# Optimization experiments

Measured on AMD Instinct MI355X. Metric: run time of the kernel, lower is better.

Reference implementation:

```python
import jax, jax.numpy as jnp
import numpy as np

N, E, B = 4096, 4096, 128  # nodes, edges, graphs


def _param(key, shape, scale):
    return jax.random.normal(key, shape, dtype=jnp.float32) * scale


def setup_inputs() -> dict:
    key = jax.random.key(0)
    ks = jax.random.split(key, 32)
    inp = {
        "x": jax.random.normal(ks[0], (N, 37), dtype=jnp.float32),
        "edge_index": jax.random.randint(ks[1], (2, E), 0, N),
        "edge_attr": jax.random.uniform(ks[2], (E, 5), dtype=jnp.float32),
        "batch": jnp.sort(jax.random.randint(ks[3], (N,), 0, B)),
        # NNConv 1: edge-MLP 5->512->37*128, root [37,128]
        "nn1_w1": _param(ks[4], (5, 512), 0.3),
        "nn1_b1": jnp.zeros((512,), jnp.float32),
        "nn1_w2": _param(ks[5], (512, 37 * 128), 0.01),
        "nn1_b2": jnp.zeros((37 * 128,), jnp.float32),
        "root1": _param(ks[6], (37, 128), 0.1),
        "bias1": jnp.zeros((128,), jnp.float32),
        # NNConv 2: edge-MLP 5->128->128*256, root [128,256]
        "nn2_w1": _param(ks[7], (5, 128), 0.3),
        "nn2_b1": jnp.zeros((128,), jnp.float32),
        "nn2_w2": _param(ks[8], (128, 128 * 256), 0.005),
        "nn2_b2": jnp.zeros((128 * 256,), jnp.float32),
        "root2": _param(ks[9], (128, 256), 0.05),
        "bias2": jnp.zeros((256,), jnp.float32),
        # NNConv 3: edge-MLP 5->128->256*256, root [256,256]
        "nn3_w1": _param(ks[10], (5, 128), 0.3),
        "nn3_b1": jnp.zeros((128,), jnp.float32),
        "nn3_w2": _param(ks[11], (128, 256 * 256), 0.005),
        "nn3_b2": jnp.zeros((256 * 256,), jnp.float32),
        "root3": _param(ks[12], (256, 256), 0.05),
        "bias3": jnp.zeros((256,), jnp.float32),
        # readout MLP
        "fc1_w": _param(ks[13], (256, 128), 0.06),
        "fc1_b": jnp.zeros((128,), jnp.float32),
        "fc2_w": _param(ks[14], (128, 64), 0.09),
        "fc2_b": jnp.zeros((64,), jnp.float32),
        "fc3_w": _param(ks[15], (64, 1), 0.12),
        "fc3_b": jnp.zeros((1,), jnp.float32),
    }
    return inp


def _nnconv(x, src, dst, edge_attr, w1, b1, w2, b2, root, bias, cin, cout):
    # edge MLP -> per-edge weight matrix [E, cin, cout]
    h = jax.nn.relu(edge_attr @ w1 + b1)
    W = (h @ w2 + b2).reshape(-1, cin, cout)
    # gather source features, per-edge matvec, scatter-add to targets
    msg = jnp.einsum('ei,eio->eo', x[src], W)          # [E, cout]
    agg = jax.ops.segment_sum(msg, dst, num_segments=x.shape[0])
    return agg + x @ root + bias


def _segment_mean(x, seg, num_segments):
    s = jax.ops.segment_sum(x, seg, num_segments=num_segments)
    cnt = jax.ops.segment_sum(jnp.ones((x.shape[0],), x.dtype), seg,
                              num_segments=num_segments)
    return s / jnp.maximum(cnt, 1.0)[:, None]


def reference(x, edge_index, edge_attr, batch,
              nn1_w1, nn1_b1, nn1_w2, nn1_b2, root1, bias1,
              nn2_w1, nn2_b1, nn2_w2, nn2_b2, root2, bias2,
              nn3_w1, nn3_b1, nn3_w2, nn3_b2, root3, bias3,
              fc1_w, fc1_b, fc2_w, fc2_b, fc3_w, fc3_b):
    src, dst = edge_index[0], edge_index[1]
    h = jax.nn.elu(_nnconv(x, src, dst, edge_attr, nn1_w1, nn1_b1, nn1_w2,
                           nn1_b2, root1, bias1, 37, 128))
    h = jax.nn.elu(_nnconv(h, src, dst, edge_attr, nn2_w1, nn2_b1, nn2_w2,
                           nn2_b2, root2, bias2, 128, 256))
    h = jax.nn.elu(_nnconv(h, src, dst, edge_attr, nn3_w1, nn3_b1, nn3_w2,
                           nn3_b2, root3, bias3, 256, 256))
    g = _segment_mean(h, batch, B)                     # [B, 256]
    g = jax.nn.elu(g @ fc1_w + fc1_b)
    g = jax.nn.elu(g @ fc2_w + fc2_b)
    g = g @ fc3_w + fc3_b
    return g.reshape(-1)
```

## Files before the change

### kernel.cpp

```cpp
#include <hip/hip_runtime.h>
#include <cstdint>
#include <cstddef>

typedef float f32x4 __attribute__((ext_vector_type(4)));
typedef _Float16 f16x8 __attribute__((ext_vector_type(8)));
typedef _Float16 f16x4 __attribute__((ext_vector_type(4)));

__device__ __forceinline__ float elu_f(float x) { return x > 0.f ? x : expm1f(x); }

__device__ __forceinline__ void gload_lds16(const void* g, void* l)
{
    __builtin_amdgcn_global_load_lds(
        (const __attribute__((address_space(1))) void*)g,
        (__attribute__((address_space(3))) void*)l,
        16, 0, 0);
}

__global__ __launch_bounds__(256)
void edge_mlp_kernel(const float* __restrict__ ea,
                     const int* __restrict__ dst, int* __restrict__ cnt,
                     const float* __restrict__ w1a, const float* __restrict__ b1a, _Float16* __restrict__ h1T,
                     const float* __restrict__ w1b, const float* __restrict__ b1b, _Float16* __restrict__ h2T,
                     const float* __restrict__ w1c, const float* __restrict__ b1c, _Float16* __restrict__ h3T,
                     int E)
{
    const int e0  = blockIdx.x * 64;
    const int tid = threadIdx.x;
    const int el  = tid & 63;
    const int cg  = tid >> 6;
    if (tid < 64) atomicAdd(&cnt[dst[e0 + tid]], 1);
    __shared__ float a[64][5];
    for (int i = tid; i < 320; i += 256) a[i / 5][i % 5] = ea[e0 * 5 + i];
    __syncthreads();
    float av[5];
    #pragma unroll
    for (int j = 0; j < 5; ++j) av[j] = a[el][j];

    #pragma unroll 4
    for (int t = 0; t < 128; ++t) {
        const int ch = t * 4 + cg;
        float s = b1a[ch];
        #pragma unroll
        for (int j = 0; j < 5; ++j) s = fmaf(av[j], w1a[j * 512 + ch], s);
        h1T[(size_t)ch * E + e0 + el] = (_Float16)fmaxf(s, 0.f);
    }
    #pragma unroll 4
    for (int t = 0; t < 32; ++t) {
        const int ch = t * 4 + cg;
        float s = b1b[ch];
        float u = b1c[ch];
        #pragma unroll
        for (int j = 0; j < 5; ++j) {
            s = fmaf(av[j], w1b[j * 128 + ch], s);
            u = fmaf(av[j], w1c[j * 128 + ch], u);
        }
        h2T[(size_t)ch * E + e0 + el] = (_Float16)fmaxf(s, 0.f);
        h3T[(size_t)ch * E + e0 + el] = (_Float16)fmaxf(u, 0.f);
    }
}

template <int CIN, int COUT, int KFTOT>
__global__ __launch_bounds__(256)
void pack_w2_kernel(const float* __restrict__ w2, const float* __restrict__ b2,
                    _Float16* __restrict__ w2h, int KH)
{
    __shared__ float tile[32][COUT + 2];
    const int bid = blockIdx.x;
    const int kh  = bid / KFTOT;
    const int c   = bid - kh * KFTOT;
    const int tid = threadIdx.x;
    const int CP  = 32 * COUT;
    for (int i = tid; i < CP; i += 256) {
        int kk = i / COUT, n = i - kk * COUT;
        int kg = c * 32 + kk;
        float v = 0.f;
        if (kg < CIN) v = (kh < KH) ? w2[((size_t)kh * CIN + kg) * COUT + n]
                                    : b2[(size_t)kg * COUT + n];
        tile[kk][n] = v;
    }
    __syncthreads();
    _Float16* outp = w2h + (size_t)bid * CP;
    for (int i = tid; i < CP; i += 256) {
        int n = i >> 5, kk = i & 31;
        int blk = (kk >> 3) ^ ((n >> 1) & 3);
        outp[n * 32 + blk * 8 + (kk & 7)] = (_Float16)tile[kk][n];
    }
}

__global__ __launch_bounds__(256)
void csr_scan_graph_kernel(const int* __restrict__ cnt, int* __restrict__ offs, int N,
                           const int* __restrict__ batch, int* __restrict__ goffs, int B,
                           int NN)
{
    __shared__ int sums[256];
    __shared__ int pref[257];
    const int tid = threadIdx.x;
    const int per = N / 256;
    int loc = 0;
    for (int i = 0; i < per; ++i) loc += cnt[tid * per + i];
    sums[tid] = loc;
    __syncthreads();
    if (tid == 0) {
        int s = 0; pref[0] = 0;
        for (int i = 0; i < 256; ++i) { s += sums[i]; pref[i + 1] = s; }
    }
    __syncthreads();
    int run = pref[tid];
    for (int i = 0; i < per; ++i) { offs[tid * per + i] = run; run += cnt[tid * per + i]; }
    if (tid == 255) offs[N] = run;
    for (int g = tid; g <= B; g += 256) {
        int lo = 0, hi = NN;
        while (lo < hi) { int mid = (lo + hi) >> 1; if (batch[mid] < g) lo = mid + 1; else hi = mid; }
        goffs[g] = lo;
    }
}

__global__ __launch_bounds__(256)
void csr_fill_kernel(const int* __restrict__ dst, const int* __restrict__ offs,
                     int* __restrict__ cur, int* __restrict__ eid, int E)
{
    int e = blockIdx.x * 256 + threadIdx.x;
    if (e < E) {
        int d = dst[e];
        int p = offs[d] + atomicAdd(&cur[d], 1);
        eid[p] = e;
    }
}

template <int KH, int CIN, int COUT, int KFTOT, int CSPLIT, int NY>
__global__ __launch_bounds__(256, 4)
void msg_mfma_kernel(const float* __restrict__ xin,
                     const _Float16* __restrict__ hT,
                     const _Float16* __restrict__ w2h,
                     const int* __restrict__ src,
                     _Float16* __restrict__ part,
                     int E, int khg_per)
{
    constexpr int BM = 128;
    constexpr int KF = KFTOT / CSPLIT;

    __shared__ __align__(16) _Float16 bsh[2][KF][64][32];
    __shared__ _Float16 s_h[2][BM];
    __shared__ int s_src[BM];

    const int tid  = threadIdx.x;
    const int lane = tid & 63;
    const int w    = tid >> 6;
    const int l15  = lane & 15;
    const int lg   = lane >> 4;
    const int swb  = (l15 >> 1) & 3;

    const int nwg = gridDim.x;
    const int bid = blockIdx.x;
    const int swz = (bid & 7) * (nwg >> 3) + (bid >> 3);
    const int m    = swz & 31;
    const int rest = swz >> 5;
    const int y    = rest % NY;
    const int zz   = rest / NY;
    const int cinH = zz % CSPLIT;
    const int zkh  = zz / CSPLIT;

    const int e0  = m * BM;
    const int n0  = y * 64;
    const int k0  = cinH * KF * 32;
    const int kh0 = zkh * khg_per;
    const int kh1 = min(kh0 + khg_per, KH + 1);

    if (tid < BM) s_src[tid] = src[e0 + tid];
    __syncthreads();

    f16x8 a_[2][KF];
    #pragma unroll
    for (int mf = 0; mf < 2; ++mf) {
        const int eloc = w * 32 + mf * 16 + l15;
        const float* xrow = xin + (size_t)s_src[eloc] * CIN + k0;
        #pragma unroll
        for (int c = 0; c < KF; ++c) {
            if (CIN % 32 == 0) {
                float4 p0 = *(const float4*)(xrow + c * 32 + lg * 8);
                float4 p1 = *(const float4*)(xrow + c * 32 + lg * 8 + 4);
                a_[mf][c][0] = (_Float16)p0.x; a_[mf][c][1] = (_Float16)p0.y;
                a_[mf][c][2] = (_Float16)p0.z; a_[mf][c][3] = (_Float16)p0.w;
                a_[mf][c][4] = (_Float16)p1.x; a_[mf][c][5] = (_Float16)p1.y;
                a_[mf][c][6] = (_Float16)p1.z; a_[mf][c][7] = (_Float16)p1.w;
            } else {
                #pragma unroll
                for (int j = 0; j < 8; ++j) {
                    int kk = c * 32 + lg * 8 + j;
                    float v = (k0 + kk < CIN) ? xrow[kk] : 0.f;
                    a_[mf][c][j] = (_Float16)v;
                }
            }
        }
    }

    f32x4 msg[2][4];
    #pragma unroll
    for (int mf = 0; mf < 2; ++mf)
        #pragma unroll
        for (int nf = 0; nf < 4; ++nf) msg[mf][nf] = 0.f;

    auto stage = [&](int khg, int pp) {
        if (khg >= kh1) return;
        const size_t chunk0 = (size_t)khg * KFTOT + cinH * KF;
        const char* g = (const char*)(w2h + (chunk0 * COUT + n0) * 32) + (size_t)tid * 16;
        char* l = (char*)(&bsh[pp][0][0][0]) + (tid >> 6) * 1024;
        #pragma unroll
        for (int c = 0; c < KF; ++c)
            gload_lds16(g + (size_t)c * COUT * 64, l + c * 4096);
    };
    auto stage_h = [&](int khg) {
        if (tid < BM && khg < kh1 && khg < KH)
            s_h[khg & 1][tid] = hT[(size_t)khg * E + e0 + tid];
    };

    int p = 0;
    stage(kh0, 0);
    stage_h(kh0);

    for (int khg = kh0; khg < kh1; ++khg) {
        __syncthreads();

        stage(khg + 1, p ^ 1);
        stage_h(khg + 1);

        _Float16 hh[2];
        #pragma unroll
        for (int mf = 0; mf < 2; ++mf)
            hh[mf] = (khg < KH) ? s_h[khg & 1][w * 32 + mf * 16 + l15] : (_Float16)1.0f;

        #pragma unroll
        for (int c = 0; c < KF; ++c) {
            f16x8 Bv[4];
            #pragma unroll
            for (int nf = 0; nf < 4; ++nf)
                Bv[nf] = *(const f16x8*)&bsh[p][c][nf * 16 + l15][(lg ^ swb) * 8];
            #pragma unroll
            for (int mf = 0; mf < 2; ++mf) {
                f16x8 ah = a_[mf][c] * hh[mf];
                #pragma unroll
                for (int nf = 0; nf < 4; ++nf)
                    msg[mf][nf] = __builtin_amdgcn_mfma_f32_16x16x32_f16(ah, Bv[nf], msg[mf][nf], 0, 0, 0);
            }
        }
        p ^= 1;
    }

    _Float16* pb = part + ((size_t)zz * E + e0) * COUT + n0;
    #pragma unroll
    for (int mf = 0; mf < 2; ++mf)
        #pragma unroll
        for (int r = 0; r < 4; ++r) {
            const int row = w * 32 + mf * 16 + lg * 4 + r;
            #pragma unroll
            for (int nf = 0; nf < 4; ++nf)
                pb[(size_t)row * COUT + nf * 16 + l15] = (_Float16)msg[mf][nf][r];
        }
}

template <int CIN, int COUT, int Z>
__global__ __launch_bounds__(256)
void node_gemm_kernel(const float* __restrict__ xin,
                      const float* __restrict__ root,
                      const _Float16* __restrict__ part,
                      const int* __restrict__ offs,
                      const int* __restrict__ eid,
                      const float* __restrict__ bias,
                      float* __restrict__ out, int E)
{
    constexpr int BM  = 64;
    constexpr int BN  = 64;
    constexpr int BKI = (CIN % 32 == 0) ? 32 : 16;
    constexpr int CIN_PAD = ((CIN + BKI - 1) / BKI) * BKI;
    constexpr int CPK = CIN_PAD / BKI;
    constexpr int NROWS = BKI / 16;

    __shared__ __align__(16) float xs_t[CIN_PAD][BM];
    __shared__ __align__(16) float btile[BKI][BN];

    const int tid = threadIdx.x;
    const int tx  = tid & 15;
    const int ty  = tid >> 4;
    const int ty4 = ty * 4;
    const int tx4 = tx * 4;
    const int e0  = blockIdx.x * BM;
    const int n0  = blockIdx.y * BN;

    for (int idx = tid; idx < BM * CIN_PAD; idx += 256) {
        int mm = idx / CIN_PAD;
        int i  = idx - mm * CIN_PAD;
        float v = 0.f;
        if (i < CIN) v = xin[(size_t)(e0 + mm) * CIN + i];
        xs_t[i][mm] = v;
    }

    const int rbase = tid >> 4;
    const int nn    = (tid & 15) * 4;
    float acc[4][4] = {};
    float4 pre[NROWS];

    {
        const float* brow = root + n0;
        #pragma unroll
        for (int rr = 0; rr < NROWS; ++rr) {
            int r = rbase + rr * 16;
            float4 v = {0.f, 0.f, 0.f, 0.f};
            if (r < CIN) v = *(const float4*)(brow + (size_t)r * COUT + nn);
            pre[rr] = v;
        }
    }

    for (int c = 0; c < CPK; ++c) {
        __syncthreads();
        #pragma unroll
        for (int rr = 0; rr < NROWS; ++rr)
            *(float4*)&btile[rbase + rr * 16][nn] = pre[rr];
        __syncthreads();

        if (c + 1 < CPK) {
            int i0n = (c + 1) * BKI;
            const float* brow = root + (size_t)i0n * COUT + n0;
            #pragma unroll
            for (int rr = 0; rr < NROWS; ++rr) {
                int r = rbase + rr * 16;
                float4 v = {0.f, 0.f, 0.f, 0.f};
                if (i0n + r < CIN) v = *(const float4*)(brow + (size_t)r * COUT + nn);
                pre[rr] = v;
            }
        }

        const int i0 = c * BKI;
        #pragma unroll
        for (int ii = 0; ii < BKI; ++ii) {
            float4 xv = *(const float4*)&xs_t[i0 + ii][ty4];
            float4 bv = *(const float4*)&btile[ii][tx4];
            float av[4] = {xv.x, xv.y, xv.z, xv.w};
            float bvv[4] = {bv.x, bv.y, bv.z, bv.w};
            #pragma unroll
            for (int mm = 0; mm < 4; ++mm)
                #pragma unroll
                for (int nq = 0; nq < 4; ++nq)
                    acc[mm][nq] = fmaf(av[mm], bvv[nq], acc[mm][nq]);
        }
    }

    float bs[4];
    #pragma unroll
    for (int nq = 0; nq < 4; ++nq) bs[nq] = bias[n0 + tx4 + nq];

    #pragma unroll
    for (int mm = 0; mm < 4; ++mm) {
        const int row = e0 + ty4 + mm;
        float add[4] = {0.f, 0.f, 0.f, 0.f};
        const int b = offs[row], t = offs[row + 1];
        for (int j = b; j < t; ++j) {
            const int e = eid[j];
            #pragma unroll
            for (int z = 0; z < Z; ++z) {
                f16x4 r4 = *(const f16x4*)(part + ((size_t)z * E + e) * COUT + n0 + tx4);
                add[0] += (float)r4.x; add[1] += (float)r4.y;
                add[2] += (float)r4.z; add[3] += (float)r4.w;
            }
        }
        size_t base = (size_t)row * COUT + n0 + tx4;
        #pragma unroll
        for (int nq = 0; nq < 4; ++nq)
            out[base + nq] = elu_f(acc[mm][nq] + add[nq] + bs[nq]);
    }
}

__global__ __launch_bounds__(256)
void pool_readout_kernel(const float* __restrict__ hl3, const int* __restrict__ goffs,
                         const float* __restrict__ fc1w, const float* __restrict__ fc1b,
                         const float* __restrict__ fc2w, const float* __restrict__ fc2b,
                         const float* __restrict__ fc3w, const float* __restrict__ fc3b,
                         float* __restrict__ outp)
{
    const int g   = blockIdx.x;
    const int tid = threadIdx.x;
    __shared__ float gm[256];
    __shared__ float a1[128];
    __shared__ float a2[64];
    const int b = goffs[g], t = goffs[g + 1];
    float s = 0.f;
    for (int n = b; n < t; ++n) s += hl3[(size_t)n * 256 + tid];
    gm[tid] = s / fmaxf((float)(t - b), 1.f);
    __syncthreads();
    if (tid < 128) {
        float v = fc1b[tid];
        for (int j = 0; j < 256; ++j) v = fmaf(gm[j], fc1w[j * 128 + tid], v);
        a1[tid] = elu_f(v);
    }
    __syncthreads();
    if (tid < 64) {
        float v = fc2b[tid];
        for (int j = 0; j < 128; ++j) v = fmaf(a1[j], fc2w[j * 64 + tid], v);
        a2[tid] = elu_f(v);
    }
    __syncthreads();
    if (tid == 0) {
        float v = fc3b[0];
        for (int j = 0; j < 64; ++j) v = fmaf(a2[j], fc3w[j], v);
        outp[g] = v;
    }
}

extern "C" void kernel_launch(void* const* d_in, const int* in_sizes, int n_in,
                              void* d_out, int out_size, void* d_ws, size_t ws_size,
                              hipStream_t stream)
{
    const float* x      = (const float*)d_in[0];
    const int*   ei     = (const int*)  d_in[1];
    const float* ea     = (const float*)d_in[2];
    const int*   batch  = (const int*)  d_in[3];
    const float* nn1_w1 = (const float*)d_in[4];
    const float* nn1_b1 = (const float*)d_in[5];
    const float* nn1_w2 = (const float*)d_in[6];
    const float* nn1_b2 = (const float*)d_in[7];
    const float* root1  = (const float*)d_in[8];
    const float* bias1  = (const float*)d_in[9];
    const float* nn2_w1 = (const float*)d_in[10];
    const float* nn2_b1 = (const float*)d_in[11];
    const float* nn2_w2 = (const float*)d_in[12];
    const float* nn2_b2 = (const float*)d_in[13];
    const float* root2  = (const float*)d_in[14];
    const float* bias2  = (const float*)d_in[15];
    const float* nn3_w1 = (const float*)d_in[16];
    const float* nn3_b1 = (const float*)d_in[17];
    const float* nn3_w2 = (const float*)d_in[18];
    const float* nn3_b2 = (const float*)d_in[19];
    const float* root3  = (const float*)d_in[20];
    const float* bias3  = (const float*)d_in[21];
    const float* fc1_w  = (const float*)d_in[22];
    const float* fc1_b  = (const float*)d_in[23];
    const float* fc2_w  = (const float*)d_in[24];
    const float* fc2_b  = (const float*)d_in[25];
    const float* fc3_w  = (const float*)d_in[26];
    const float* fc3_b  = (const float*)d_in[27];

    const int E = in_sizes[2] / 5;
    const int N = in_sizes[0] / 37;
    const int B = out_size;
    const int* srcp = ei;
    const int* dstp = ei + E;

    const size_t W1H = (size_t)513 * 2 * 128 * 32;
    const size_t W2H = (size_t)129 * 4 * 256 * 32;
    const size_t W3H = (size_t)129 * 8 * 256 * 32;
    _Float16* w2h1 = (_Float16*)d_ws;
    _Float16* w2h2 = w2h1 + W1H;
    _Float16* w2h3 = w2h2 + W2H;
    _Float16* h1T  = w2h3 + W3H;
    _Float16* h2T  = h1T + (size_t)512 * E;
    _Float16* h3T  = h2T + (size_t)128 * E;
    _Float16* part = h3T + (size_t)128 * E;
    float* fbase = (float*)(part + (size_t)16 * E * 128);
    float* hl1   = fbase;
    float* hl2   = hl1 + (size_t)N * 128;
    float* hl3   = hl2 + (size_t)N * 256;
    int* ibase   = (int*)(hl3 + (size_t)N * 256);
    int* cnt   = ibase;
    int* cur   = cnt + N;
    int* offs  = cur + N;
    int* eid   = offs + N + 1;
    int* goffs = eid + E;

    hipMemsetAsync(cnt, 0, 2 * N * sizeof(int), stream);

    edge_mlp_kernel<<<E / 64, 256, 0, stream>>>(ea, dstp, cnt,
                                                nn1_w1, nn1_b1, h1T,
                                                nn2_w1, nn2_b1, h2T,
                                                nn3_w1, nn3_b1, h3T, E);

    pack_w2_kernel<37, 128, 2><<<513 * 2, 256, 0, stream>>>(nn1_w2, nn1_b2, w2h1, 512);
    pack_w2_kernel<128, 256, 4><<<129 * 4, 256, 0, stream>>>(nn2_w2, nn2_b2, w2h2, 128);
    pack_w2_kernel<256, 256, 8><<<129 * 8, 256, 0, stream>>>(nn3_w2, nn3_b2, w2h3, 128);

    csr_scan_graph_kernel<<<1, 256, 0, stream>>>(cnt, offs, N, batch, goffs, B, N);
    csr_fill_kernel<<<(E + 255) / 256, 256, 0, stream>>>(dstp, offs, cur, eid, E);

    msg_mfma_kernel<512, 37, 128, 2, 1, 2><<<1024, 256, 0, stream>>>(
        x, h1T, w2h1, srcp, part, E, 33);
    node_gemm_kernel<37, 128, 16><<<dim3(N / 64, 2), 256, 0, stream>>>(
        x, root1, part, offs, eid, bias1, hl1, E);

    msg_mfma_kernel<128, 128, 256, 4, 1, 4><<<1024, 256, 0, stream>>>(
        hl1, h2T, w2h2, srcp, part, E, 17);
    node_gemm_kernel<128, 256, 8><<<dim3(N / 64, 4), 256, 0, stream>>>(
        hl1, root2, part, offs, eid, bias2, hl2, E);

    msg_mfma_kernel<128, 256, 256, 8, 2, 4><<<1024, 256, 0, stream>>>(
        hl2, h3T, w2h3, srcp, part, E, 33);
    node_gemm_kernel<256, 256, 8><<<dim3(N / 64, 4), 256, 0, stream>>>(
        hl2, root3, part, offs, eid, bias3, hl3, E);

    pool_readout_kernel<<<B, 256, 0, stream>>>(hl3, goffs, fc1_w, fc1_b,
                                               fc2_w, fc2_b, fc3_w, fc3_b,
                                               (float*)d_out);
}
```

Baseline: 312.4 us.

## Use 32x32 MFMA with two-stage K batching and bf16x3 MFMA node GEMM

```diff
diff --git a/kernel.cpp b/kernel.cpp
--- a/kernel.cpp
+++ b/kernel.cpp
@@ -2,11 +2,19 @@
 #include <cstdint>
 #include <cstddef>
 
-typedef float f32x4 __attribute__((ext_vector_type(4)));
+typedef float f32x16 __attribute__((ext_vector_type(16)));
 typedef _Float16 f16x8 __attribute__((ext_vector_type(8)));
-typedef _Float16 f16x4 __attribute__((ext_vector_type(4)));
+typedef short s16x8 __attribute__((ext_vector_type(8)));
 
 __device__ __forceinline__ float elu_f(float x) { return x > 0.f ? x : expm1f(x); }
+
+__device__ __forceinline__ unsigned short f2bf(float f) {
+    unsigned u = __float_as_uint(f);
+    return (unsigned short)((u + 0x7FFFu + ((u >> 16) & 1u)) >> 16);
+}
+__device__ __forceinline__ float bf2f(unsigned short b) {
+    return __uint_as_float(((unsigned)b) << 16);
+}
 
 __device__ __forceinline__ void gload_lds16(const void* g, void* l)
 {
@@ -128,7 +136,7 @@
 }
 
 template <int KH, int CIN, int COUT, int KFTOT, int CSPLIT, int NY>
-__global__ __launch_bounds__(256, 4)
+__global__ __launch_bounds__(256, 2)
 void msg_mfma_kernel(const float* __restrict__ xin,
                      const _Float16* __restrict__ hT,
                      const _Float16* __restrict__ w2h,
@@ -138,17 +146,17 @@
 {
     constexpr int BM = 128;
     constexpr int KF = KFTOT / CSPLIT;
-
-    __shared__ __align__(16) _Float16 bsh[2][KF][64][32];
-    __shared__ _Float16 s_h[2][BM];
+    constexpr int KS = KF * 2;
+
+    __shared__ __align__(16) _Float16 bsh[2][2][KF][64][32];
+    __shared__ _Float16 s_h[2][2][BM];
     __shared__ int s_src[BM];
 
     const int tid  = threadIdx.x;
     const int lane = tid & 63;
     const int w    = tid >> 6;
-    const int l15  = lane & 15;
-    const int lg   = lane >> 4;
-    const int swb  = (l15 >> 1) & 3;
+    const int l31  = lane & 31;
+    const int hi   = lane >> 5;
 
     const int nwg = gridDim.x;
     const int bid = blockIdx.x;
@@ -169,78 +177,79 @@
     if (tid < BM) s_src[tid] = src[e0 + tid];
     __syncthreads();
 
-    f16x8 a_[2][KF];
-    #pragma unroll
-    for (int mf = 0; mf < 2; ++mf) {
-        const int eloc = w * 32 + mf * 16 + l15;
-        const float* xrow = xin + (size_t)s_src[eloc] * CIN + k0;
-        #pragma unroll
-        for (int c = 0; c < KF; ++c) {
+    f16x8 a_[KS];
+    {
+        const int row = w * 32 + l31;
+        const float* xrow = xin + (size_t)s_src[row] * CIN + k0;
+        #pragma unroll
+        for (int ks = 0; ks < KS; ++ks) {
             if (CIN % 32 == 0) {
-                float4 p0 = *(const float4*)(xrow + c * 32 + lg * 8);
-                float4 p1 = *(const float4*)(xrow + c * 32 + lg * 8 + 4);
-                a_[mf][c][0] = (_Float16)p0.x; a_[mf][c][1] = (_Float16)p0.y;
-                a_[mf][c][2] = (_Float16)p0.z; a_[mf][c][3] = (_Float16)p0.w;
-                a_[mf][c][4] = (_Float16)p1.x; a_[mf][c][5] = (_Float16)p1.y;
-                a_[mf][c][6] = (_Float16)p1.z; a_[mf][c][7] = (_Float16)p1.w;
+                float4 p0 = *(const float4*)(xrow + ks * 16 + hi * 8);
+                float4 p1 = *(const float4*)(xrow + ks * 16 + hi * 8 + 4);
+                a_[ks][0] = (_Float16)p0.x; a_[ks][1] = (_Float16)p0.y;
+                a_[ks][2] = (_Float16)p0.z; a_[ks][3] = (_Float16)p0.w;
+                a_[ks][4] = (_Float16)p1.x; a_[ks][5] = (_Float16)p1.y;
+                a_[ks][6] = (_Float16)p1.z; a_[ks][7] = (_Float16)p1.w;
             } else {
                 #pragma unroll
                 for (int j = 0; j < 8; ++j) {
-                    int kk = c * 32 + lg * 8 + j;
+                    int kk = ks * 16 + hi * 8 + j;
                     float v = (k0 + kk < CIN) ? xrow[kk] : 0.f;
-                    a_[mf][c][j] = (_Float16)v;
+                    a_[ks][j] = (_Float16)v;
                 }
             }
         }
     }
 
-    f32x4 msg[2][4];
-    #pragma unroll
-    for (int mf = 0; mf < 2; ++mf)
-        #pragma unroll
-        for (int nf = 0; nf < 4; ++nf) msg[mf][nf] = 0.f;
-
-    auto stage = [&](int khg, int pp) {
-        if (khg >= kh1) return;
-        const size_t chunk0 = (size_t)khg * KFTOT + cinH * KF;
-        const char* g = (const char*)(w2h + (chunk0 * COUT + n0) * 32) + (size_t)tid * 16;
-        char* l = (char*)(&bsh[pp][0][0][0]) + (tid >> 6) * 1024;
-        #pragma unroll
-        for (int c = 0; c < KF; ++c)
-            gload_lds16(g + (size_t)c * COUT * 64, l + c * 4096);
+    f32x16 acc[2];
+    acc[0] = 0.f; acc[1] = 0.f;
+
+    auto stage2 = [&](int kb, int pp) {
+        #pragma unroll
+        for (int sub = 0; sub < 2; ++sub) {
+            const int kh = kb + sub;
+            if (kh >= kh1) break;
+            const char* g = (const char*)(w2h + ((size_t)(kh * KFTOT + cinH * KF) * COUT + n0) * 32)
+                          + (size_t)tid * 16;
+            char* l = (char*)(&bsh[pp][sub][0][0][0]) + (tid >> 6) * 1024;
+            #pragma unroll
+            for (int c = 0; c < KF; ++c)
+                gload_lds16(g + (size_t)c * COUT * 64, l + c * 4096);
+        }
     };
-    auto stage_h = [&](int khg) {
-        if (tid < BM && khg < kh1 && khg < KH)
-            s_h[khg & 1][tid] = hT[(size_t)khg * E + e0 + tid];
+    auto stage_h2 = [&](int kb, int pp) {
+        const int sub = tid >> 7;
+        const int idx = tid & 127;
+        const int kh = kb + sub;
+        if (kh < kh1 && kh < KH) s_h[pp][sub][idx] = hT[(size_t)kh * E + e0 + idx];
     };
 
     int p = 0;
-    stage(kh0, 0);
-    stage_h(kh0);
-
-    for (int khg = kh0; khg < kh1; ++khg) {
+    stage2(kh0, 0);
+    stage_h2(kh0, 0);
+
+    for (int kb = kh0; kb < kh1; kb += 2) {
         __syncthreads();
 
-        stage(khg + 1, p ^ 1);
-        stage_h(khg + 1);
-
-        _Float16 hh[2];
-        #pragma unroll
-        for (int mf = 0; mf < 2; ++mf)
-            hh[mf] = (khg < KH) ? s_h[khg & 1][w * 32 + mf * 16 + l15] : (_Float16)1.0f;
-
-        #pragma unroll
-        for (int c = 0; c < KF; ++c) {
-            f16x8 Bv[4];
+        stage2(kb + 2, p ^ 1);
+        stage_h2(kb + 2, p ^ 1);
+
+        #pragma unroll
+        for (int sub = 0; sub < 2; ++sub) {
+            const int kh = kb + sub;
+            if (kh >= kh1) break;
+            const _Float16 hh = (kh < KH) ? s_h[p][sub][w * 32 + l31] : (_Float16)1.0f;
             #pragma unroll
-            for (int nf = 0; nf < 4; ++nf)
-                Bv[nf] = *(const f16x8*)&bsh[p][c][nf * 16 + l15][(lg ^ swb) * 8];
-            #pragma unroll
-            for (int mf = 0; mf < 2; ++mf) {
-                f16x8 ah = a_[mf][c] * hh[mf];
+            for (int ks = 0; ks < KS; ++ks) {
+                const int c = ks >> 1;
+                const f16x8 ah = a_[ks] * hh;
                 #pragma unroll
-                for (int nf = 0; nf < 4; ++nf)
-                    msg[mf][nf] = __builtin_amdgcn_mfma_f32_16x16x32_f16(ah, Bv[nf], msg[mf][nf], 0, 0, 0);
+                for (int nf = 0; nf < 2; ++nf) {
+                    const int n = nf * 32 + l31;
+                    const int blk = (((ks & 1) * 2 + hi) ^ ((n >> 1) & 3));
+                    const f16x8 Bv = *(const f16x8*)((const char*)(&bsh[p][sub][c][n][0]) + blk * 16);
+                    acc[nf] = __builtin_amdgcn_mfma_f32_32x32x16_f16(ah, Bv, acc[nf], 0, 0, 0);
+                }
             }
         }
         p ^= 1;
@@ -248,19 +257,17 @@
 
     _Float16* pb = part + ((size_t)zz * E + e0) * COUT + n0;
     #pragma unroll
-    for (int mf = 0; mf < 2; ++mf)
-        #pragma unroll
-        for (int r = 0; r < 4; ++r) {
-            const int row = w * 32 + mf * 16 + lg * 4 + r;
-            #pragma unroll
-            for (int nf = 0; nf < 4; ++nf)
-                pb[(size_t)row * COUT + nf * 16 + l15] = (_Float16)msg[mf][nf][r];
-        }
-}
-
-template <int CIN, int COUT, int Z>
-__global__ __launch_bounds__(256)
-void node_gemm_kernel(const float* __restrict__ xin,
+    for (int nf = 0; nf < 2; ++nf)
+        #pragma unroll
+        for (int r = 0; r < 16; ++r) {
+            const int row = w * 32 + (r & 3) + 8 * (r >> 2) + 4 * hi;
+            pb[(size_t)row * COUT + nf * 32 + l31] = (_Float16)acc[nf][r];
+        }
+}
+
+template <int CIN, int COUT, int Z, int KP>
+__global__ __launch_bounds__(256, 1)
+void node_mfma_kernel(const float* __restrict__ xin,
                       const float* __restrict__ root,
                       const _Float16* __restrict__ part,
                       const int* __restrict__ offs,
@@ -268,104 +275,88 @@
                       const float* __restrict__ bias,
                       float* __restrict__ out, int E)
 {
-    constexpr int BM  = 64;
-    constexpr int BN  = 64;
-    constexpr int BKI = (CIN % 32 == 0) ? 32 : 16;
-    constexpr int CIN_PAD = ((CIN + BKI - 1) / BKI) * BKI;
-    constexpr int CPK = CIN_PAD / BKI;
-    constexpr int NROWS = BKI / 16;
-
-    __shared__ __align__(16) float xs_t[CIN_PAD][BM];
-    __shared__ __align__(16) float btile[BKI][BN];
-
-    const int tid = threadIdx.x;
-    const int tx  = tid & 15;
-    const int ty  = tid >> 4;
-    const int ty4 = ty * 4;
-    const int tx4 = tx * 4;
-    const int e0  = blockIdx.x * BM;
-    const int n0  = blockIdx.y * BN;
-
-    for (int idx = tid; idx < BM * CIN_PAD; idx += 256) {
-        int mm = idx / CIN_PAD;
-        int i  = idx - mm * CIN_PAD;
-        float v = 0.f;
-        if (i < CIN) v = xin[(size_t)(e0 + mm) * CIN + i];
-        xs_t[i][mm] = v;
-    }
-
-    const int rbase = tid >> 4;
-    const int nn    = (tid & 15) * 4;
-    float acc[4][4] = {};
-    float4 pre[NROWS];
-
-    {
-        const float* brow = root + n0;
-        #pragma unroll
-        for (int rr = 0; rr < NROWS; ++rr) {
-            int r = rbase + rr * 16;
-            float4 v = {0.f, 0.f, 0.f, 0.f};
-            if (r < CIN) v = *(const float4*)(brow + (size_t)r * COUT + nn);
-            pre[rr] = v;
-        }
-    }
-
-    for (int c = 0; c < CPK; ++c) {
-        __syncthreads();
-        #pragma unroll
-        for (int rr = 0; rr < NROWS; ++rr)
-            *(float4*)&btile[rbase + rr * 16][nn] = pre[rr];
-        __syncthreads();
-
-        if (c + 1 < CPK) {
-            int i0n = (c + 1) * BKI;
-            const float* brow = root + (size_t)i0n * COUT + n0;
+    constexpr int KB = KP / 8;
+    __shared__ __align__(16) short ash[2][64][KP];
+    __shared__ __align__(16) short bsh[2][64][KP];
+
+    const int tid  = threadIdx.x;
+    const int lane = tid & 63;
+    const int w    = tid >> 6;
+    const int l31  = lane & 31;
+    const int hi   = lane >> 5;
+    const int m0   = blockIdx.x * 64;
+    const int n0   = blockIdx.y * 64;
+
+    for (int b = tid; b < 64 * KB; b += 256) {
+        const int n = b / KB, kb = b - n * KB;
+        float v[8];
+        if (CIN == KP) {
+            float4 p0 = *(const float4*)(xin + (size_t)(m0 + n) * CIN + kb * 8);
+            float4 p1 = *(const float4*)(xin + (size_t)(m0 + n) * CIN + kb * 8 + 4);
+            v[0] = p0.x; v[1] = p0.y; v[2] = p0.z; v[3] = p0.w;
+            v[4] = p1.x; v[5] = p1.y; v[6] = p1.z; v[7] = p1.w;
+        } else {
             #pragma unroll
-            for (int rr = 0; rr < NROWS; ++rr) {
-                int r = rbase + rr * 16;
-                float4 v = {0.f, 0.f, 0.f, 0.f};
-                if (i0n + r < CIN) v = *(const float4*)(brow + (size_t)r * COUT + nn);
-                pre[rr] = v;
+            for (int j = 0; j < 8; ++j) {
+                int k = kb * 8 + j;
+                v[j] = (k < CIN) ? xin[(size_t)(m0 + n) * CIN + k] : 0.f;
             }
         }
-
-        const int i0 = c * BKI;
-        #pragma unroll
-        for (int ii = 0; ii < BKI; ++ii) {
-            float4 xv = *(const float4*)&xs_t[i0 + ii][ty4];
-            float4 bv = *(const float4*)&btile[ii][tx4];
-            float av[4] = {xv.x, xv.y, xv.z, xv.w};
-            float bvv[4] = {bv.x, bv.y, bv.z, bv.w};
-            #pragma unroll
-            for (int mm = 0; mm < 4; ++mm)
-                #pragma unroll
-                for (int nq = 0; nq < 4; ++nq)
-                    acc[mm][nq] = fmaf(av[mm], bvv[nq], acc[mm][nq]);
-        }
-    }
-
-    float bs[4];
+        s16x8 h8, l8;
+        #pragma unroll
+        for (int j = 0; j < 8; ++j) {
+            unsigned short hb = f2bf(v[j]);
+            h8[j] = (short)hb;
+            l8[j] = (short)f2bf(v[j] - bf2f(hb));
+        }
+        const int d = (kb ^ (n & 7)) * 8;
+        *(s16x8*)&ash[0][n][d] = h8;
+        *(s16x8*)&ash[1][n][d] = l8;
+    }
+    for (int b = tid; b < 64 * KP; b += 256) {
+        const int k = b >> 6, n = b & 63;
+        float v = (k < CIN) ? root[(size_t)k * COUT + n0 + n] : 0.f;
+        unsigned short hb = f2bf(v);
+        unsigned short lb = f2bf(v - bf2f(hb));
+        const int d = ((k >> 3) ^ (n & 7)) * 8 + (k & 7);
+        bsh[0][n][d] = (short)hb;
+        bsh[1][n][d] = (short)lb;
+    }
+    __syncthreads();
+
+    const int wr = w >> 1, wc = w & 1;
+    const int an = wr * 32 + l31;
+    const int bn = wc * 32 + l31;
+    f32x16 ahh, alh, ahl;
+    ahh = 0.f; alh = 0.f; ahl = 0.f;
+
     #pragma unroll
-    for (int nq = 0; nq < 4; ++nq) bs[nq] = bias[n0 + tx4 + nq];
-
+    for (int ks = 0; ks < KP / 16; ++ks) {
+        const int kb_ = ks * 2 + hi;
+        const s16x8 Ah = *(const s16x8*)&ash[0][an][(kb_ ^ (an & 7)) * 8];
+        const s16x8 Al = *(const s16x8*)&ash[1][an][(kb_ ^ (an & 7)) * 8];
+        const s16x8 Bh = *(const s16x8*)&bsh[0][bn][(kb_ ^ (bn & 7)) * 8];
+        const s16x8 Bl = *(const s16x8*)&bsh[1][bn][(kb_ ^ (bn & 7)) * 8];
+        ahh = __builtin_amdgcn_mfma_f32_32x32x16_bf16(Ah, Bh, ahh, 0, 0, 0);
+        alh = __builtin_amdgcn_mfma_f32_32x32x16_bf16(Al, Bh, alh, 0, 0, 0);
+        ahl = __builtin_amdgcn_mfma_f32_32x32x16_bf16(Ah, Bl, ahl, 0, 0, 0);
+    }
+
+    const int colg = n0 + wc * 32 + l31;
+    const float bv = bias[colg];
     #pragma unroll
-    for (int mm = 0; mm < 4; ++mm) {
-        const int row = e0 + ty4 + mm;
-        float add[4] = {0.f, 0.f, 0.f, 0.f};
+    for (int r = 0; r < 16; ++r) {
+        const int row = m0 + wr * 32 + (r & 3) + 8 * (r >> 2) + 4 * hi;
+        float v = ahh[r] + alh[r] + ahl[r];
+        float add = 0.f;
         const int b = offs[row], t = offs[row + 1];
         for (int j = b; j < t; ++j) {
             const int e = eid[j];
             #pragma unroll
-            for (int z = 0; z < Z; ++z) {
-                f16x4 r4 = *(const f16x4*)(part + ((size_t)z * E + e) * COUT + n0 + tx4);
-                add[0] += (float)r4.x; add[1] += (float)r4.y;
-                add[2] += (float)r4.z; add[3] += (float)r4.w;
-            }
-        }
-        size_t base = (size_t)row * COUT + n0 + tx4;
-        #pragma unroll
-        for (int nq = 0; nq < 4; ++nq)
-            out[base + nq] = elu_f(acc[mm][nq] + add[nq] + bs[nq]);
+            for (int z = 0; z < Z; ++z)
+                add += (float)part[((size_t)z * E + e) * COUT + colg];
+        }
+        out[(size_t)row * COUT + colg] = elu_f(v + add + bv);
     }
 }
 
@@ -481,17 +472,17 @@
 
     msg_mfma_kernel<512, 37, 128, 2, 1, 2><<<1024, 256, 0, stream>>>(
         x, h1T, w2h1, srcp, part, E, 33);
-    node_gemm_kernel<37, 128, 16><<<dim3(N / 64, 2), 256, 0, stream>>>(
+    node_mfma_kernel<37, 128, 16, 64><<<dim3(64, 2), 256, 0, stream>>>(
         x, root1, part, offs, eid, bias1, hl1, E);
 
     msg_mfma_kernel<128, 128, 256, 4, 1, 4><<<1024, 256, 0, stream>>>(
         hl1, h2T, w2h2, srcp, part, E, 17);
-    node_gemm_kernel<128, 256, 8><<<dim3(N / 64, 4), 256, 0, stream>>>(
+    node_mfma_kernel<128, 256, 8, 128><<<dim3(64, 4), 256, 0, stream>>>(
         hl1, root2, part, offs, eid, bias2, hl2, E);
 
     msg_mfma_kernel<128, 256, 256, 8, 2, 4><<<1024, 256, 0, stream>>>(
         hl2, h3T, w2h3, srcp, part, E, 33);
-    node_gemm_kernel<256, 256, 8><<<dim3(N / 64, 4), 256, 0, stream>>>(
+    node_mfma_kernel<256, 256, 8, 256><<<dim3(64, 4), 256, 0, stream>>>(
         hl2, root3, part, offs, eid, bias3, hl3, E);
 
     pool_readout_kernel<<<B, 256, 0, stream>>>(hl3, goffs, fc1_w, fc1_b,
```

After: 363.2 us. 16.3% more time.
